# Kernel tuning notes

Measured on AMD Instinct MI355X. Metric: run time of the kernel, lower is better.

Reference implementation:

```python
import jax, jax.numpy as jnp
import numpy as np

N_NODES = 50000
N_EDGES = 1600000
IN_FEATS = 128
HIDDEN = 16
HEADS = 8
SLOPE = 0.2


def setup_inputs() -> dict:
    key = jax.random.key(0)
    ks = jax.random.split(key, 9)
    feat = jax.random.normal(ks[0], (N_NODES, IN_FEATS), dtype=jnp.float32)
    edge_src = jax.random.randint(ks[1], (N_EDGES,), 0, N_NODES, dtype=jnp.int32)
    edge_dst = jax.random.randint(ks[2], (N_EDGES,), 0, N_NODES, dtype=jnp.int32)
    # layer 0: in=128 -> H*F=128 ; layer 1: in=128 (concat of layer 0) -> 128
    s0 = 1.0 / np.sqrt(IN_FEATS)
    W0 = jax.random.normal(ks[3], (IN_FEATS, HEADS * HIDDEN), dtype=jnp.float32) * s0
    al0 = jax.random.normal(ks[4], (HEADS, HIDDEN), dtype=jnp.float32) * 0.1
    ar0 = jax.random.normal(ks[5], (HEADS, HIDDEN), dtype=jnp.float32) * 0.1
    W1 = jax.random.normal(ks[6], (HEADS * HIDDEN, HEADS * HIDDEN), dtype=jnp.float32) * s0
    al1 = jax.random.normal(ks[7], (HEADS, HIDDEN), dtype=jnp.float32) * 0.1
    ar1 = jax.random.normal(ks[8], (HEADS, HIDDEN), dtype=jnp.float32) * 0.1
    return {"feat": feat, "edge_src": edge_src, "edge_dst": edge_dst,
            "W0": W0, "al0": al0, "ar0": ar0, "W1": W1, "al1": al1, "ar1": ar1}


def _gat_conv(feat, W, al, ar, src, dst):
    """One DGL-style GATConv: no bias, no residual, no dropout, no activation."""
    n = feat.shape[0]
    h = (feat @ W).reshape(n, HEADS, HIDDEN)              # [N,H,F]
    el = jnp.sum(h * al, axis=-1)                          # [N,H]
    er = jnp.sum(h * ar, axis=-1)                          # [N,H]
    e = jax.nn.leaky_relu(el[src] + er[dst], negative_slope=SLOPE)  # [E,H]
    # edge softmax over incoming edges of each dst node
    m = jax.ops.segment_max(e, dst, num_segments=n)        # [N,H]
    ex = jnp.exp(e - m[dst])                               # [E,H]
    denom = jax.ops.segment_sum(ex, dst, num_segments=n)   # [N,H]
    alpha = ex / jnp.where(denom[dst] > 0, denom[dst], 1.0)
    # message passing: gather src features, weight, scatter-add to dst
    out = jax.ops.segment_sum(h[src] * alpha[:, :, None], dst, num_segments=n)
    return out                                             # [N,H,F]


def reference(feat, edge_src, edge_dst, W0, al0, ar0, W1, al1, ar1):
    n = feat.shape[0]
    # step 1 + concat (flatten heads)
    x = _gat_conv(feat, W0, al0, ar0, edge_src, edge_dst).reshape(n, HEADS * HIDDEN)
    # step 2 + concat
    x = _gat_conv(x, W1, al1, ar1, edge_src, edge_dst).reshape(n, HEADS * HIDDEN)
    return x
```

## Files before the change

### kernel.cpp

```cpp
#include <hip/hip_runtime.h>
#include <hip/hip_bf16.h>


#define HEADS 8
#define HID 16
#define HF 128
#define SLOPE 0.2f

#define BSHIFT 8
#define BRANGE 256
#define CHUNK 4096

typedef __attribute__((ext_vector_type(8))) short bf16x8;
typedef __attribute__((ext_vector_type(4))) float f32x4;

static __device__ __forceinline__ unsigned int f2bf(float f) {
    unsigned int u = __float_as_uint(f);
    u += 0x7fffu + ((u >> 16) & 1u);
    return u >> 16;
}


template <bool XBF16>
static __device__ __forceinline__ void gemm_body(
    int blk, unsigned short* xs, unsigned short* ws,
    const void* __restrict__ Xv, const unsigned short* __restrict__ Wtb,
    const float* __restrict__ AL, const float* __restrict__ AR,
    unsigned short* __restrict__ Hb, float* __restrict__ EL,
    float* __restrict__ ER, int n) {
    int t = threadIdx.x;
    int row0 = blk * 64;

    {
        int r = t >> 2;
        int gr = row0 + r;
        unsigned int rowbase = r * 256;
        unsigned int sw = (r & 7) << 4;
        if (XBF16) {
            unsigned int kb0 = (t & 3) * 64;
            const char* src = (const char*)Xv + (size_t)gr * 256 + kb0;
            #pragma unroll
            for (int i = 0; i < 4; ++i) {
                int4 v = (gr < n) ? *(const int4*)(src + i * 16)
                                  : make_int4(0, 0, 0, 0);
                *(int4*)((char*)xs + rowbase + ((kb0 + i * 16) ^ sw)) = v;
            }
        } else {
            int k0 = (t & 3) * 32;
            float4 f[8];
            if (gr < n) {
                const float4* p = (const float4*)((const float*)Xv + (size_t)gr * HF + k0);
                #pragma unroll
                for (int i = 0; i < 8; ++i) f[i] = p[i];
            } else {
                #pragma unroll
                for (int i = 0; i < 8; ++i) f[i] = make_float4(0.f, 0.f, 0.f, 0.f);
            }
            #pragma unroll
            for (int g2 = 0; g2 < 4; ++g2) {
                float4 a = f[g2 * 2], b = f[g2 * 2 + 1];
                int4 pk;
                pk.x = (int)(f2bf(a.x) | (f2bf(a.y) << 16));
                pk.y = (int)(f2bf(a.z) | (f2bf(a.w) << 16));
                pk.z = (int)(f2bf(b.x) | (f2bf(b.y) << 16));
                pk.w = (int)(f2bf(b.z) | (f2bf(b.w) << 16));
                unsigned int addr = rowbase + ((unsigned)((k0 + g2 * 8) * 2) ^ sw);
                *(int4*)((char*)xs + addr) = pk;
            }
        }
    }
    {
        int c = t >> 1;
        unsigned int kb0 = (t & 1) * 128;
        const int4* src = (const int4*)((const char*)Wtb + (size_t)c * 256 + kb0);
        unsigned int sw = (c & 7) << 4;
        #pragma unroll
        for (int i = 0; i < 8; ++i) {
            int4 v = src[i];
            unsigned int addr = c * 256 + ((kb0 + i * 16) ^ sw);
            *(int4*)((char*)ws + addr) = v;
        }
    }
    __syncthreads();

    int wv = t >> 6;
    int l = t & 63;
    int lr = l & 15;
    int g = l >> 4;

    bf16x8 bfr[4];
    {
        int r = wv * 16 + lr;
        unsigned int rowbase = r * 256;
        unsigned int sw = (r & 7) << 4;
        #pragma unroll
        for (int s = 0; s < 4; ++s) {
            unsigned int kbyte = (unsigned)((s * 32 + g * 8) * 2);
            bfr[s] = *(bf16x8*)((char*)xs + rowbase + (kbyte ^ sw));
        }
    }

    f32x4 acc[8];
    #pragma unroll
    for (int ct = 0; ct < 8; ++ct) acc[ct] = (f32x4){0.f, 0.f, 0.f, 0.f};

    #pragma unroll
    for (int ct = 0; ct < 8; ++ct) {
        int c = ct * 16 + lr;
        unsigned int rowbase = c * 256;
        unsigned int sw = (c & 7) << 4;
        #pragma unroll
        for (int s = 0; s < 4; ++s) {
            unsigned int kbyte = (unsigned)((s * 32 + g * 8) * 2);
            bf16x8 af = *(bf16x8*)((char*)ws + rowbase + (kbyte ^ sw));
            acc[ct] = __builtin_amdgcn_mfma_f32_16x16x32_bf16(af, bfr[s], acc[ct], 0, 0, 0);
        }
    }

    int grow = row0 + wv * 16 + lr;
    bool valid = grow < n;

    if (valid) {
        #pragma unroll
        for (int ct = 0; ct < 8; ++ct) {
            ushort4 hb4 = make_ushort4(
                (unsigned short)f2bf(acc[ct][0]), (unsigned short)f2bf(acc[ct][1]),
                (unsigned short)f2bf(acc[ct][2]), (unsigned short)f2bf(acc[ct][3]));
            *(ushort4*)(Hb + (size_t)grow * HF + ct * 16 + g * 4) = hb4;
        }
    }

    #pragma unroll
    for (int ct = 0; ct < 8; ++ct) {
        float e1 = 0.f, e2 = 0.f;
        #pragma unroll
        for (int rg = 0; rg < 4; ++rg) {
            float alv = AL[ct * 16 + g * 4 + rg];
            float arv = AR[ct * 16 + g * 4 + rg];
            e1 += acc[ct][rg] * alv;
            e2 += acc[ct][rg] * arv;
        }
        e1 += __shfl_xor(e1, 16); e1 += __shfl_xor(e1, 32);
        e2 += __shfl_xor(e2, 16); e2 += __shfl_xor(e2, 32);
        if (g == 0 && valid) {
            EL[grow * HEADS + ct] = e1;
            ER[grow * HEADS + ct] = e2;
        }
    }
}


static __device__ __forceinline__ void wtrans_body(
    int blk, const float* __restrict__ W, unsigned short* __restrict__ Wtb) {
    int gid = blk * 256 + threadIdx.x;
    int c = gid >> 3;
    int k0 = (gid & 7) * 16;
    #pragma unroll
    for (int q = 0; q < 4; ++q) {
        int k = k0 + q * 4;
        ushort4 o = make_ushort4(
            (unsigned short)f2bf(W[(k + 0) * HF + c]),
            (unsigned short)f2bf(W[(k + 1) * HF + c]),
            (unsigned short)f2bf(W[(k + 2) * HF + c]),
            (unsigned short)f2bf(W[(k + 3) * HF + c]));
        *(ushort4*)(Wtb + (size_t)c * HF + k) = o;
    }
}


static __device__ __forceinline__ void csr_body(
    int b, char* ldsc, const int* __restrict__ stage, const int* __restrict__ btot,
    int* __restrict__ rowptr, unsigned short* __restrict__ col,
    int N, int nb, int E) {
    int* hist  = (int*)ldsc;
    int* lscan = hist + 256;
    int* lcur  = lscan + 256;
    int* sb    = lcur + 256;
    int t = threadIdx.x;
    sb[t] = (t < nb) ? btot[t] : 0;
    hist[t] = 0;
    __syncthreads();
    #pragma unroll
    for (int off = 1; off < 256; off <<= 1) {
        int v = (t >= off) ? sb[t - off] : 0;
        __syncthreads();
        sb[t] += v;
        __syncthreads();
    }
    int e0 = (b == 0) ? 0 : sb[b - 1];
    int e1 = sb[b];
    if (b == 0 && t == 0) rowptr[N] = E;

    for (int i = e0 + t; i < e1; i += 256)
        atomicAdd(&hist[(stage[i] >> 16) & (BRANGE - 1)], 1);
    __syncthreads();
    lscan[t] = hist[t];
    __syncthreads();
    #pragma unroll
    for (int off = 1; off < 256; off <<= 1) {
        int v = (t >= off) ? lscan[t - off] : 0;
        __syncthreads();
        lscan[t] += v;
        __syncthreads();
    }
    int ex = (t == 0) ? 0 : lscan[t - 1];
    __syncthreads();
    lcur[t] = ex;
    int node = (b << BSHIFT) + t;
    if (node < N) rowptr[node] = e0 + ex;
    __syncthreads();
    for (int i = e0 + t; i < e1; i += 256) {
        int p = stage[i];
        int pos = e0 + atomicAdd(&lcur[(p >> 16) & (BRANGE - 1)], 1);
        col[pos] = (unsigned short)(p & 0xFFFF);
    }
}


__global__ __launch_bounds__(256) void fused_pre_kernel(
    const int* __restrict__ edst, int* __restrict__ bhistT, int E, int nb, int nblk,
    const float* __restrict__ W0, unsigned short* __restrict__ wtb0,
    const float* __restrict__ W1, unsigned short* __restrict__ wtb1) {
    __shared__ int h[BRANGE];
    int b = blockIdx.x;
    int t = threadIdx.x;
    if (b < nblk) {
        h[t] = 0;
        __syncthreads();
        int base = b * CHUNK;
        int end = base + CHUNK; if (end > E) end = E;
        for (int i = base + t; i < end; i += 256)
            atomicAdd(&h[edst[i] >> BSHIFT], 1);
        __syncthreads();
        if (t < nb) bhistT[(size_t)t * nblk + b] = h[t];
    } else if (b < nblk + 4) {
        wtrans_body(b - nblk, W0, wtb0);
    } else {
        wtrans_body(b - nblk - 4, W1, wtb1);
    }
}

__global__ __launch_bounds__(64) void bscan1_kernel(
    const int* __restrict__ bhistT, int* __restrict__ boffT,
    int* __restrict__ btot, int nblk) {
    int b = blockIdx.x;
    int l = threadIdx.x;
    int carry = 0;
    for (int c0 = 0; c0 < nblk; c0 += 64) {
        int blk = c0 + l;
        int v = (blk < nblk) ? bhistT[(size_t)b * nblk + blk] : 0;
        int x = v;
        #pragma unroll
        for (int off = 1; off < 64; off <<= 1) {
            int y = __shfl_up(x, off, 64);
            if (l >= off) x += y;
        }
        if (blk < nblk) boffT[(size_t)b * nblk + blk] = carry + x - v;
        carry += __shfl(x, 63);
    }
    if (l == 0) btot[b] = carry;
}

__global__ __launch_bounds__(512) void bucket_scatter_kernel(
    const int* __restrict__ src, const int* __restrict__ dst,
    const int* __restrict__ bhistT, const int* __restrict__ boffT,
    const int* __restrict__ btot, int* __restrict__ stage,
    int E, int nb, int nblk) {
    __shared__ int lscan[BRANGE];
    __shared__ int lcur[BRANGE];
    __shared__ int gbase[BRANGE];
    __shared__ int sb[BRANGE];
    __shared__ int sstage[CHUNK];
    int t = threadIdx.x;
    int blk = blockIdx.x;
    int base = blk * CHUNK;
    int end = base + CHUNK; if (end > E) end = E;

    if (t < 256) {
        lscan[t] = (t < nb) ? bhistT[(size_t)t * nblk + blk] : 0;
        sb[t] = (t < nb) ? btot[t] : 0;
    }
    __syncthreads();
    #pragma unroll
    for (int off = 1; off < 256; off <<= 1) {
        int v = 0, u = 0;
        if (t < 256 && t >= off) { v = lscan[t - off]; u = sb[t - off]; }
        __syncthreads();
        if (t < 256) { lscan[t] += v; sb[t] += u; }
        __syncthreads();
    }
    int ex = 0;
    if (t < 256) ex = (t == 0) ? 0 : lscan[t - 1];
    __syncthreads();
    if (t < 256) {
        lcur[t] = ex;
        lscan[t] = ex;
        if (t < nb) {
            int bb = (t == 0) ? 0 : sb[t - 1];
            gbase[t] = bb + boffT[(size_t)t * nblk + blk];
        }
    }
    __syncthreads();

    for (int i = base + t; i < end; i += 512) {
        int d = dst[i];
        int b = d >> BSHIFT;
        int pos = atomicAdd(&lcur[b], 1);
        sstage[pos] = (src[i] & 0xFFFF) | ((d & (BRANGE - 1)) << 16) | (b << 24);
    }
    __syncthreads();

    int total = end - base;
    for (int i = t; i < total; i += 512) {
        int p = sstage[i];
        int b = ((unsigned)p) >> 24;
        int gpos = gbase[b] + (i - lscan[b]);
        stage[gpos] = p;
    }
}


__global__ __launch_bounds__(256) void fused_mid_kernel(
    const int* __restrict__ stage, const int* __restrict__ btot,
    int* __restrict__ rowptr, unsigned short* __restrict__ col,
    int N, int nb, int E, int nCsr,
    const float* __restrict__ X, const unsigned short* __restrict__ wtb0,
    const float* __restrict__ AL, const float* __restrict__ AR,
    unsigned short* __restrict__ Hb, float* __restrict__ EL,
    float* __restrict__ ER) {
    __shared__ __align__(16) unsigned char lds[48 * 1024];
    int b = blockIdx.x;
    if (b < nCsr) {
        csr_body(b, (char*)lds, stage, btot, rowptr, col, N, nb, E);
    } else {
        gemm_body<false>(b - nCsr, (unsigned short*)lds,
                         (unsigned short*)(lds + 16384),
                         X, wtb0, AL, AR, Hb, EL, ER, N);
    }
}


template <bool XBF16>
__global__ __launch_bounds__(256) void gemm_mfma_kernel(
    const void* __restrict__ Xv, const unsigned short* __restrict__ Wtb,
    const float* __restrict__ AL, const float* __restrict__ AR,
    unsigned short* __restrict__ Hb, float* __restrict__ EL,
    float* __restrict__ ER, int n) {
    __shared__ __align__(16) unsigned short xs[64 * HF];
    __shared__ __align__(16) unsigned short ws[HF * HF];
    gemm_body<XBF16>(blockIdx.x, xs, ws, Xv, Wtb, AL, AR, Hb, EL, ER, n);
}


template <bool OBF16>
__global__ __launch_bounds__(256) void gat_aggregate_kernel(
    const unsigned int* __restrict__ HbU,
    const float* __restrict__ EL, const float* __restrict__ ER,
    const int* __restrict__ rowptr, const unsigned short* __restrict__ col,
    void* __restrict__ OUT, int n) {
    int wid = (int)((blockIdx.x * blockDim.x + threadIdx.x) >> 6);
    if (wid >= n) return;
    int lane = threadIdx.x & 63;
    int s0 = rowptr[wid], s1 = rowptr[wid + 1];
    if (s1 == s0) {
        if (OBF16) ((unsigned int*)OUT)[(size_t)wid * 64 + lane] = 0u;
        else ((float2*)OUT)[(size_t)wid * 64 + lane] = make_float2(0.f, 0.f);
        return;
    }

    int h = lane & 7;
    int j = lane >> 3;
    int hC = lane >> 3;
    float er_h = ER[wid * HEADS + h];

    float accx = 0.f, accy = 0.f;
    float dpart = 0.f;

    for (int base = s0; base < s1; base += 8) {
        int i = base + j;
        int icl = i < s1 ? i : s1 - 1;
        int sj = (int)col[icl];
        float e = EL[sj * HEADS + h] + er_h;
        e = fmaxf(e, SLOPE * e);
        float w = __expf(e);
        if (i >= s1) w = 0.f;
        dpart += w;

        if (base + 8 <= s1) {
            #pragma unroll
            for (int jj = 0; jj < 8; ++jj) {
                float wC = __shfl(w, jj * 8 + hC);
                int s = __builtin_amdgcn_readlane(sj, jj * 8);
                unsigned int pv = HbU[(size_t)s * 64 + lane];
                accx += wC * __uint_as_float(pv << 16);
                accy += wC * __uint_as_float(pv & 0xffff0000u);
            }
        } else {
            int ne = s1 - base;
            for (int jj = 0; jj < ne; ++jj) {
                float wC = __shfl(w, jj * 8 + hC);
                int s = __builtin_amdgcn_readlane(sj, jj * 8);
                unsigned int pv = HbU[(size_t)s * 64 + lane];
                accx += wC * __uint_as_float(pv << 16);
                accy += wC * __uint_as_float(pv & 0xffff0000u);
            }
        }
    }

    dpart += __shfl_xor(dpart, 8);
    dpart += __shfl_xor(dpart, 16);
    dpart += __shfl_xor(dpart, 32);
    float rC = 1.f / __shfl(dpart, hC);

    if (OBF16) {
        unsigned int o = f2bf(accx * rC) | (f2bf(accy * rC) << 16);
        ((unsigned int*)OUT)[(size_t)wid * 64 + lane] = o;
    } else {
        ((float2*)OUT)[(size_t)wid * 64 + lane] = make_float2(accx * rC, accy * rC);
    }
}


extern "C" void kernel_launch(void* const* d_in, const int* in_sizes, int n_in,
                              void* d_out, int out_size, void* d_ws, size_t ws_size,
                              hipStream_t stream) {
    const float* feat = (const float*)d_in[0];
    const int*   esrc = (const int*)d_in[1];
    const int*   edst = (const int*)d_in[2];
    const float* W0   = (const float*)d_in[3];
    const float* al0  = (const float*)d_in[4];
    const float* ar0  = (const float*)d_in[5];
    const float* W1   = (const float*)d_in[6];
    const float* al1  = (const float*)d_in[7];
    const float* ar1  = (const float*)d_in[8];
    float* out = (float*)d_out;

    const int N = in_sizes[0] / HF;
    const int E = in_sizes[1];
    const int nb = (N + BRANGE - 1) >> BSHIFT;
    const int nblk = (E + CHUNK - 1) / CHUNK;

    char* w = (char*)d_ws;
    auto alloc = [&](size_t bytes) -> void* {
        void* p = (void*)w;
        w += (bytes + 255) & ~(size_t)255;
        return p;
    };
    unsigned short* hb   = (unsigned short*)alloc((size_t)N * HF * 2);
    unsigned short* x1b  = (unsigned short*)alloc((size_t)N * HF * 2);
    float* el_buf = (float*)alloc((size_t)N * HEADS * 4);
    float* er_buf = (float*)alloc((size_t)N * HEADS * 4);
    int*   rowptr = (int*)alloc((size_t)(N + 1) * 4);
    unsigned short* col = (unsigned short*)alloc((size_t)E * 2);
    int*   bhistT = (int*)alloc((size_t)nb * nblk * 4);
    int*   boffT  = (int*)alloc((size_t)nb * nblk * 4);
    int*   btot   = (int*)alloc((size_t)nb * 4);
    unsigned short* wtb0 = (unsigned short*)alloc((size_t)HF * HF * 2);
    unsigned short* wtb1 = (unsigned short*)alloc((size_t)HF * HF * 2);
    int*   stage  = (int*)alloc((size_t)E * 4);

    int gGemm = (N + 63) / 64;
    int gAgg  = (N * 64 + 255) / 256;

    fused_pre_kernel<<<nblk + 8, 256, 0, stream>>>(edst, bhistT, E, nb, nblk,
                                                   W0, wtb0, W1, wtb1);
    bscan1_kernel<<<nb, 64, 0, stream>>>(bhistT, boffT, btot, nblk);
    bucket_scatter_kernel<<<nblk, 512, 0, stream>>>(esrc, edst, bhistT, boffT,
                                                    btot, stage, E, nb, nblk);
    fused_mid_kernel<<<nb + gGemm, 256, 0, stream>>>(
        stage, btot, rowptr, col, N, nb, E, nb,
        feat, wtb0, al0, ar0, hb, el_buf, er_buf);

    gat_aggregate_kernel<true><<<gAgg, 256, 0, stream>>>(
        (const unsigned int*)hb, el_buf, er_buf, rowptr, col, x1b, N);

    gemm_mfma_kernel<true><<<gGemm, 256, 0, stream>>>(x1b, wtb1, al1, ar1,
                                                      hb, el_buf, er_buf, N);
    gat_aggregate_kernel<false><<<gAgg, 256, 0, stream>>>(
        (const unsigned int*)hb, el_buf, er_buf, rowptr, col, out, N);
}
```

Measured before the change: 211.3 us.

## Split layer-0 GEMM blocks between bucket-scatter and CSR-build launches

The bucket scatter kernel is merged with the first 352 blocks of the layer-0 feature GEMM into one launch, and the remaining GEMM blocks stay co-scheduled with the CSR build. The scatter path drops from 512 to 256 threads per block and uses a shared 48KB LDS buffer. This spreads the GEMM work so it runs alongside both graph-preprocessing phases, hiding more of its cost behind the latency-bound scatter. The risk is that halving scatter threads makes each scatter block slower, and the fixed split of 352 GEMM blocks may unbalance the two launches.

New measurement: 214.4 us. About the same (+1.5%).

```diff
diff --git a/kernel.cpp b/kernel.cpp
--- a/kernel.cpp
+++ b/kernel.cpp
@@ -168,6 +168,57 @@
 }
 
 
+static __device__ __forceinline__ void scatter_body(
+    int blk, char* ldsc,
+    const int* __restrict__ src, const int* __restrict__ dst,
+    const int* __restrict__ bhistT, const int* __restrict__ boffT,
+    const int* __restrict__ btot, int* __restrict__ stage,
+    int E, int nb, int nblk) {
+    int* lscan  = (int*)ldsc;
+    int* lcur   = lscan + 256;
+    int* gbase  = lcur + 256;
+    int* sb     = gbase + 256;
+    int* sstage = sb + 256;
+    int t = threadIdx.x;
+    int base = blk * CHUNK;
+    int end = base + CHUNK; if (end > E) end = E;
+
+    lscan[t] = (t < nb) ? bhistT[(size_t)t * nblk + blk] : 0;
+    sb[t]    = (t < nb) ? btot[t] : 0;
+    __syncthreads();
+    #pragma unroll
+    for (int off = 1; off < 256; off <<= 1) {
+        int v = (t >= off) ? lscan[t - off] : 0;
+        int u = (t >= off) ? sb[t - off] : 0;
+        __syncthreads();
+        lscan[t] += v; sb[t] += u;
+        __syncthreads();
+    }
+    int ex = (t == 0) ? 0 : lscan[t - 1];
+    int bb = (t == 0) ? 0 : sb[t - 1];
+    __syncthreads();
+    lcur[t] = ex;
+    lscan[t] = ex;
+    if (t < nb) gbase[t] = bb + boffT[(size_t)t * nblk + blk];
+    __syncthreads();
+
+    for (int i = base + t; i < end; i += 256) {
+        int d = dst[i];
+        int b = d >> BSHIFT;
+        int pos = atomicAdd(&lcur[b], 1);
+        sstage[pos] = (src[i] & 0xFFFF) | ((d & (BRANGE - 1)) << 16) | (b << 24);
+    }
+    __syncthreads();
+
+    int total = end - base;
+    for (int i = t; i < total; i += 256) {
+        int p = sstage[i];
+        int b = ((unsigned)p) >> 24;
+        stage[gbase[b] + (i - lscan[b])] = p;
+    }
+}
+
+
 static __device__ __forceinline__ void csr_body(
     int b, char* ldsc, const int* __restrict__ stage, const int* __restrict__ btot,
     int* __restrict__ rowptr, unsigned short* __restrict__ col,
@@ -261,61 +312,24 @@
     if (l == 0) btot[b] = carry;
 }
 
-__global__ __launch_bounds__(512) void bucket_scatter_kernel(
+
+__global__ __launch_bounds__(256) void fused_scatter_kernel(
     const int* __restrict__ src, const int* __restrict__ dst,
     const int* __restrict__ bhistT, const int* __restrict__ boffT,
     const int* __restrict__ btot, int* __restrict__ stage,
-    int E, int nb, int nblk) {
-    __shared__ int lscan[BRANGE];
-    __shared__ int lcur[BRANGE];
-    __shared__ int gbase[BRANGE];
-    __shared__ int sb[BRANGE];
-    __shared__ int sstage[CHUNK];
-    int t = threadIdx.x;
-    int blk = blockIdx.x;
-    int base = blk * CHUNK;
-    int end = base + CHUNK; if (end > E) end = E;
-
-    if (t < 256) {
-        lscan[t] = (t < nb) ? bhistT[(size_t)t * nblk + blk] : 0;
-        sb[t] = (t < nb) ? btot[t] : 0;
-    }
-    __syncthreads();
-    #pragma unroll
-    for (int off = 1; off < 256; off <<= 1) {
-        int v = 0, u = 0;
-        if (t < 256 && t >= off) { v = lscan[t - off]; u = sb[t - off]; }
-        __syncthreads();
-        if (t < 256) { lscan[t] += v; sb[t] += u; }
-        __syncthreads();
-    }
-    int ex = 0;
-    if (t < 256) ex = (t == 0) ? 0 : lscan[t - 1];
-    __syncthreads();
-    if (t < 256) {
-        lcur[t] = ex;
-        lscan[t] = ex;
-        if (t < nb) {
-            int bb = (t == 0) ? 0 : sb[t - 1];
-            gbase[t] = bb + boffT[(size_t)t * nblk + blk];
-        }
-    }
-    __syncthreads();
-
-    for (int i = base + t; i < end; i += 512) {
-        int d = dst[i];
-        int b = d >> BSHIFT;
-        int pos = atomicAdd(&lcur[b], 1);
-        sstage[pos] = (src[i] & 0xFFFF) | ((d & (BRANGE - 1)) << 16) | (b << 24);
-    }
-    __syncthreads();
-
-    int total = end - base;
-    for (int i = t; i < total; i += 512) {
-        int p = sstage[i];
-        int b = ((unsigned)p) >> 24;
-        int gpos = gbase[b] + (i - lscan[b]);
-        stage[gpos] = p;
+    int E, int nb, int nblk,
+    const float* __restrict__ X, const unsigned short* __restrict__ wtb0,
+    const float* __restrict__ AL, const float* __restrict__ AR,
+    unsigned short* __restrict__ Hb, float* __restrict__ EL,
+    float* __restrict__ ER, int N) {
+    __shared__ __align__(16) unsigned char lds[48 * 1024];
+    int b = blockIdx.x;
+    if (b < nblk) {
+        scatter_body(b, (char*)lds, src, dst, bhistT, boffT, btot, stage, E, nb, nblk);
+    } else {
+        gemm_body<false>(b - nblk, (unsigned short*)lds,
+                         (unsigned short*)(lds + 16384),
+                         X, wtb0, AL, AR, Hb, EL, ER, N);
     }
 }
 
@@ -323,7 +337,7 @@
 __global__ __launch_bounds__(256) void fused_mid_kernel(
     const int* __restrict__ stage, const int* __restrict__ btot,
     int* __restrict__ rowptr, unsigned short* __restrict__ col,
-    int N, int nb, int E, int nCsr,
+    int N, int nb, int E, int nCsr, int gSplit,
     const float* __restrict__ X, const unsigned short* __restrict__ wtb0,
     const float* __restrict__ AL, const float* __restrict__ AR,
     unsigned short* __restrict__ Hb, float* __restrict__ EL,
@@ -333,7 +347,7 @@
     if (b < nCsr) {
         csr_body(b, (char*)lds, stage, btot, rowptr, col, N, nb, E);
     } else {
-        gemm_body<false>(b - nCsr, (unsigned short*)lds,
+        gemm_body<false>(b - nCsr + gSplit, (unsigned short*)lds,
                          (unsigned short*)(lds + 16384),
                          X, wtb0, AL, AR, Hb, EL, ER, N);
     }
@@ -460,15 +474,17 @@
     int*   stage  = (int*)alloc((size_t)E * 4);
 
     int gGemm = (N + 63) / 64;
+    int gSplit = 352;
     int gAgg  = (N * 64 + 255) / 256;
 
     fused_pre_kernel<<<nblk + 8, 256, 0, stream>>>(edst, bhistT, E, nb, nblk,
                                                    W0, wtb0, W1, wtb1);
     bscan1_kernel<<<nb, 64, 0, stream>>>(bhistT, boffT, btot, nblk);
-    bucket_scatter_kernel<<<nblk, 512, 0, stream>>>(esrc, edst, bhistT, boffT,
-                                                    btot, stage, E, nb, nblk);
-    fused_mid_kernel<<<nb + gGemm, 256, 0, stream>>>(
-        stage, btot, rowptr, col, N, nb, E, nb,
+    fused_scatter_kernel<<<nblk + gSplit, 256, 0, stream>>>(
+        esrc, edst, bhistT, boffT, btot, stage, E, nb, nblk,
+        feat, wtb0, al0, ar0, hb, el_buf, er_buf, N);
+    fused_mid_kernel<<<nb + (gGemm - gSplit), 256, 0, stream>>>(
+        stage, btot, rowptr, col, N, nb, E, nb, gSplit,
         feat, wtb0, al0, ar0, hb, el_buf, er_buf);
 
     gat_aggregate_kernel<true><<<gAgg, 256, 0, stream>>>(
```
